# Kernel optimization log

Hardware: AMD Instinct MI355X
Metric: run time of the kernel (lower is better)

The kernel has to match this reference:

```python
import jax, jax.numpy as jnp
import numpy as np
import math

SCALES = (1, 2, 4, 8)


def interp1d(x, L_out):
    """F.interpolate(mode='linear', align_corners=False) along last axis."""
    L_in = x.shape[-1]
    if L_in == L_out:
        return x
    scale = L_in / L_out
    src = (jnp.arange(L_out, dtype=jnp.float32) + 0.5) * scale - 0.5
    src = jnp.clip(src, 0.0, float(L_in - 1))
    i0 = jnp.floor(src).astype(jnp.int32)
    i1 = jnp.minimum(i0 + 1, L_in - 1)
    w1 = (src - i0.astype(jnp.float32)).astype(x.dtype)
    return x[..., i0] * (1.0 - w1) + x[..., i1] * w1


def setup_inputs() -> dict:
    key = jax.random.key(0)
    ks = jax.random.split(key, 5)
    B, H, S, D = 2, 16, 1024, 64
    query = jax.random.normal(ks[0], (B, H, S, D), jnp.float32)
    k = jax.random.normal(ks[1], (B, H, S, D), jnp.float32)
    v = jax.random.normal(ks[2], (B, H, S, D), jnp.float32)
    # 4 per-scale Linear(head_dim, head_dim): W[i] is [out, in] (torch layout), b[i] is [out]
    W = jax.random.normal(ks[3], (len(SCALES), D, D), jnp.float32) * (1.0 / np.sqrt(D))
    b = jax.random.normal(ks[4], (len(SCALES), D), jnp.float32) * 0.01
    return {"query": query, "key": k, "value": v, "W": W, "b": b}


def reference(query, key, value, W, b):
    B, H, S, D = query.shape
    inv_sqrt_d = 1.0 / math.sqrt(D)
    outs, probs_all = [], []
    for i, s in enumerate(SCALES):
        if s > 1:
            # avg_pool1d(kernel=stride=s) over the sequence axis
            pk = key.reshape(B, H, S // s, s, D).mean(axis=3)
            pv = value.reshape(B, H, S // s, s, D).mean(axis=3)
        else:
            pk, pv = key, value
        # per-scale linear projection of pooled keys (torch Linear: x @ W.T + b)
        proj = jnp.einsum('bhkd,ed->bhke', pk, W[i]) + b[i]
        scores = jnp.einsum('bhqd,bhkd->bhqk', query, proj) * inv_sqrt_d
        probs = jax.nn.softmax(scores, axis=-1)  # [B,H,S,S//s]
        if s > 1:
            # upsample attn probs along key axis, and pooled values along seq axis
            probs = interp1d(probs, S)                               # [B,H,S,S]
            pv = jnp.swapaxes(interp1d(jnp.swapaxes(pv, -1, -2), S), -1, -2)  # [B,H,S,D]
        outs.append(jnp.einsum('bhqk,bhkd->bhqd', probs, pv))
        probs_all.append(probs)
    combined_output = jnp.stack(outs).mean(axis=0)
    combined_attention = jnp.stack(probs_all).mean(axis=0)
    return combined_output, combined_attention
```

## Files before the change

### kernel.cpp

```cpp
#include <hip/hip_runtime.h>

#define S_LEN 1024
#define DH 64
#define NBH 32
#define CROWS 1920
#define HEAD_K (CROWS * DH)
#define NCHUNK (HEAD_K / 8)
#define ATTN_OFF (NBH * S_LEN * DH)
#define PSTR 1928

typedef __attribute__((ext_vector_type(8))) short bf8_t;
typedef __attribute__((ext_vector_type(4))) float f32x4_t;

__device__ __forceinline__ unsigned short f2bf(float x) {
  unsigned u = __float_as_uint(x);
  u += 0x7fffu + ((u >> 16) & 1u);
  return (unsigned short)(u >> 16);
}
__device__ __forceinline__ float bf2f(unsigned short h) {
  return __uint_as_float(((unsigned)h) << 16);
}

__global__ __launch_bounds__(256, 3) void prep_kernel(
    const float* __restrict__ key, const float* __restrict__ value,
    const float* __restrict__ W, const float* __restrict__ b,
    unsigned short* __restrict__ projB, unsigned short* __restrict__ mpvB)
{
  __shared__ __align__(16) float Wl[64 * 64];
  __shared__ __align__(16) float pkv[68 * 68];
  __shared__ __align__(16) float prL[64 * 68];
  __shared__ float coefs[64 * 4];
  const int t = threadIdx.x;
  const int bid = blockIdx.x;
  const int bh = bid / 30;
  const int tt = bid % 30;
  int si, jt;
  if (tt < 16)      { si = 0; jt = tt; }
  else if (tt < 24) { si = 1; jt = tt - 16; }
  else if (tt < 28) { si = 2; jt = tt - 24; }
  else              { si = 3; jt = tt - 28; }
  const int s = 1 << si;
  const int L = 1024 >> si;
  const int off = (si == 0) ? 0 : (si == 1) ? 1024 : (si == 2) ? 1536 : 1792;
  const int j0 = jt << 6;
  const float invs = 1.0f / (float)s;

  for (int i = t; i < 1024; i += 256)
    *(float4*)&Wl[i * 4] = *(const float4*)&W[si * 4096 + i * 4];

  const float* Kp = key + bh * (S_LEN * DH);
  for (int i = t; i < 1024; i += 256) {
    const int j = i >> 4, d4 = (i & 15) << 2;
    const float* src = Kp + (j0 + j) * s * DH + d4;
    float4 a = {0.f, 0.f, 0.f, 0.f};
    for (int f = 0; f < s; f++) {
      const float4 kv = *(const float4*)(src + f * DH);
      a.x += kv.x; a.y += kv.y; a.z += kv.z; a.w += kv.w;
    }
    a.x *= invs; a.y *= invs; a.z *= invs; a.w *= invs;
    *(float4*)&pkv[j * 68 + d4] = a;
  }

  if (t < 64) {
    const int j = j0 + t;
    float cm = 0.f, cc = 0.f, cp = 0.f;
    const int klo = max(0, (j - 1) * s);
    const int khi = min(S_LEN - 1, (j + 2) * s);
    for (int kf = klo; kf <= khi; kf++) {
      float srcp = ((float)kf + 0.5f) * invs - 0.5f;
      srcp = fminf(fmaxf(srcp, 0.f), (float)(L - 1));
      const int i0 = (int)floorf(srcp);
      const int i1 = min(i0 + 1, L - 1);
      const float w = srcp - (float)i0;
      float u = 0.f;
      if (i0 == j) u += 1.f - w;
      if (i1 == j) u += w;
      if (u != 0.f) {
        const float g0 = u * (1.f - w), g1 = u * w;
        if (i0 == j) cc += g0; else cm += g0;
        if (i1 == j) cc += g1; else cp += g1;
      }
    }
    coefs[t * 4 + 0] = cm; coefs[t * 4 + 1] = cc; coefs[t * 4 + 2] = cp;
  }
  __syncthreads();

  {
    const int j  = t & 63;
    const int e0 = (t >> 6) << 4;
    float acc[16];
    #pragma unroll
    for (int ee = 0; ee < 16; ee++) acc[ee] = b[si * 64 + e0 + ee];
    #pragma unroll
    for (int dq = 0; dq < 16; dq++) {
      const float4 p4 = *(const float4*)&pkv[j * 68 + dq * 4];
      #pragma unroll
      for (int ee = 0; ee < 16; ee++) {
        const float4 w4 = *(const float4*)&Wl[(e0 + ee) * 64 + dq * 4];
        acc[ee] += p4.x * w4.x + p4.y * w4.y + p4.z * w4.z + p4.w * w4.w;
      }
    }
    #pragma unroll
    for (int ee = 0; ee < 16; ee++) prL[j * 68 + e0 + ee] = acc[ee];
  }
  __syncthreads();

  const float* Vp = value + bh * (S_LEN * DH);
  for (int i = t; i < 1088; i += 256) {
    const int hj = i >> 4, d4 = (i & 15) << 2;
    const int jg = min(max(j0 - 2 + hj, 0), L - 1);
    const float* src = Vp + jg * s * DH + d4;
    float4 a = {0.f, 0.f, 0.f, 0.f};
    for (int f = 0; f < s; f++) {
      const float4 vv = *(const float4*)(src + f * DH);
      a.x += vv.x; a.y += vv.y; a.z += vv.z; a.w += vv.w;
    }
    a.x *= invs; a.y *= invs; a.z *= invs; a.w *= invs;
    *(float4*)&pkv[hj * 68 + d4] = a;
  }

  const int ktg0 = (off + j0) >> 4;
  for (int c = t; c < 512; c += 256) {
    const int ktl = c >> 7;
    const int db  = (c >> 6) & 1;
    const int ln  = c & 63;
    const int kl  = ktl * 16 + (ln & 15);
    const int e0p = db * 32 + ((ln >> 4) & 3) * 8;
    const float4 a  = *(const float4*)&prL[kl * 68 + e0p];
    const float4 c4 = *(const float4*)&prL[kl * 68 + e0p + 4];
    bf8_t v;
    v[0] = (short)f2bf(a.x);  v[1] = (short)f2bf(a.y);
    v[2] = (short)f2bf(a.z);  v[3] = (short)f2bf(a.w);
    v[4] = (short)f2bf(c4.x); v[5] = (short)f2bf(c4.y);
    v[6] = (short)f2bf(c4.z); v[7] = (short)f2bf(c4.w);
    ((bf8_t*)projB)[bh * NCHUNK + ((ktg0 + ktl) * 2 + db) * 64 + ln] = v;
  }
  __syncthreads();

  const int kbg0 = (off + j0) >> 5;
  for (int c = t; c < 512; c += 256) {
    const int kbl = c >> 8;
    const int nt  = (c >> 6) & 3;
    const int ln  = c & 63;
    const int d   = nt * 16 + (ln & 15);
    const int r0  = kbl * 32 + ((ln >> 4) & 3) * 8;
    bf8_t v;
    #pragma unroll
    for (int jj = 0; jj < 8; jj++) {
      const int rl = r0 + jj;
      const float cm = coefs[rl * 4 + 0];
      const float cc = coefs[rl * 4 + 1];
      const float cp = coefs[rl * 4 + 2];
      const float val = cm * pkv[(rl + 1) * 68 + d] +
                        cc * pkv[(rl + 2) * 68 + d] +
                        cp * pkv[(rl + 3) * 68 + d];
      v[jj] = (short)f2bf(val);
    }
    ((bf8_t*)mpvB)[bh * NCHUNK + ((kbg0 + kbl) * 4 + nt) * 64 + ln] = v;
  }
}

__global__ __launch_bounds__(256, 2) void fused_attn_kernel(
    const float* __restrict__ query, const unsigned short* __restrict__ projB,
    const unsigned short* __restrict__ mpvB, float* __restrict__ out)
{
  __shared__ __align__(16) unsigned short prbf[16 * PSTR];
  const int t    = threadIdx.x;
  const int bh   = blockIdx.x & 31;
  const int qt   = blockIdx.x >> 5;
  const int q0   = qt << 4;
  const int wave = t >> 6;
  const int lane = t & 63;
  const int quad = lane >> 4;
  const int n16  = lane & 15;

  bf8_t af0, af1;
  {
    const float* qrow = query + bh * (S_LEN * DH) + (q0 + n16) * DH;
    const float4 a0 = *(const float4*)(qrow + quad * 8);
    const float4 a1 = *(const float4*)(qrow + quad * 8 + 4);
    const float4 a2 = *(const float4*)(qrow + 32 + quad * 8);
    const float4 a3 = *(const float4*)(qrow + 32 + quad * 8 + 4);
    af0[0] = (short)f2bf(a0.x); af0[1] = (short)f2bf(a0.y);
    af0[2] = (short)f2bf(a0.z); af0[3] = (short)f2bf(a0.w);
    af0[4] = (short)f2bf(a1.x); af0[5] = (short)f2bf(a1.y);
    af0[6] = (short)f2bf(a1.z); af0[7] = (short)f2bf(a1.w);
    af1[0] = (short)f2bf(a2.x); af1[1] = (short)f2bf(a2.y);
    af1[2] = (short)f2bf(a2.z); af1[3] = (short)f2bf(a2.w);
    af1[4] = (short)f2bf(a3.x); af1[5] = (short)f2bf(a3.y);
    af1[6] = (short)f2bf(a3.z); af1[7] = (short)f2bf(a3.w);
  }

  {
    const bf8_t* pB = (const bf8_t*)projB + bh * NCHUNK;
    for (int kt = wave; kt < 120; kt += 4) {
      const bf8_t b0 = pB[(kt * 2 + 0) * 64 + lane];
      const bf8_t b1 = pB[(kt * 2 + 1) * 64 + lane];
      f32x4_t c = {0.f, 0.f, 0.f, 0.f};
      c = __builtin_amdgcn_mfma_f32_16x16x32_bf16(af0, b0, c, 0, 0, 0);
      c = __builtin_amdgcn_mfma_f32_16x16x32_bf16(af1, b1, c, 0, 0, 0);
      const int col = kt * 16 + n16;
      #pragma unroll
      for (int i = 0; i < 4; i++)
        prbf[(quad * 4 + i) * PSTR + col] = f2bf(c[i] * 0.125f);
    }
  }
  __syncthreads();

  {
    const int rr = t >> 4;
    const int g  = t & 15;
    unsigned short* prr = prbf + rr * PSTR;
    #pragma unroll
    for (int si = 0; si < 4; si++) {
      const int L   = 1024 >> si;
      const int off = (si == 0) ? 0 : (si == 1) ? 1024 : (si == 2) ? 1536 : 1792;
      const int nch = L >> 2;
      float m = -1e30f;
      for (int ch = g; ch < nch; ch += 16) {
        const ushort4 u = *(const ushort4*)(prr + off + ch * 4);
        m = fmaxf(m, fmaxf(fmaxf(bf2f(u.x), bf2f(u.y)),
                           fmaxf(bf2f(u.z), bf2f(u.w))));
      }
      #pragma unroll
      for (int dlt = 8; dlt >= 1; dlt >>= 1) m = fmaxf(m, __shfl_xor(m, dlt));
      float ssum = 0.f;
      for (int ch = g; ch < nch; ch += 16) {
        ushort4 u = *(const ushort4*)(prr + off + ch * 4);
        const float e0 = __expf(bf2f(u.x) - m);
        const float e1 = __expf(bf2f(u.y) - m);
        const float e2 = __expf(bf2f(u.z) - m);
        const float e3 = __expf(bf2f(u.w) - m);
        ssum += (e0 + e1) + (e2 + e3);
        u.x = f2bf(e0); u.y = f2bf(e1); u.z = f2bf(e2); u.w = f2bf(e3);
        *(ushort4*)(prr + off + ch * 4) = u;
      }
      #pragma unroll
      for (int dlt = 8; dlt >= 1; dlt >>= 1) ssum += __shfl_xor(ssum, dlt);
      const float inv = 1.0f / ssum;
      for (int ch = g; ch < nch; ch += 16) {
        ushort4 u = *(const ushort4*)(prr + off + ch * 4);
        u.x = f2bf(bf2f(u.x) * inv); u.y = f2bf(bf2f(u.y) * inv);
        u.z = f2bf(bf2f(u.z) * inv); u.w = f2bf(bf2f(u.w) * inv);
        *(ushort4*)(prr + off + ch * 4) = u;
      }
    }
  }
  __syncthreads();

  {
    const bf8_t* pM = (const bf8_t*)mpvB + bh * NCHUNK;
    f32x4_t acc = {0.f, 0.f, 0.f, 0.f};
    for (int kb = 0; kb < 60; kb++) {
      const bf8_t a = *(const bf8_t*)(prbf + n16 * PSTR + kb * 32 + quad * 8);
      const bf8_t bb = pM[(kb * 4 + wave) * 64 + lane];
      acc = __builtin_amdgcn_mfma_f32_16x16x32_bf16(a, bb, acc, 0, 0, 0);
    }
    float* ob = out + bh * (S_LEN * DH) + q0 * DH;
    #pragma unroll
    for (int i = 0; i < 4; i++)
      ob[(quad * 4 + i) * DH + wave * 16 + n16] = acc[i] * 0.25f;
  }

  float* ab = out + ATTN_OFF + (size_t)bh * (S_LEN * S_LEN) + (size_t)q0 * S_LEN;
  for (int rep = 0; rep < 16; rep++) {
    const int idx = rep * 256 + t;
    const int rr  = idx >> 8;
    const int k0  = (idx & 255) << 2;
    const unsigned short* p2 = prbf + rr * PSTR;
    const ushort4 bs = *(const ushort4*)(p2 + k0);
    float res[4] = {bf2f(bs.x), bf2f(bs.y), bf2f(bs.z), bf2f(bs.w)};
    #pragma unroll
    for (int si = 1; si < 4; si++) {
      const int   L     = 1024 >> si;
      const int   off2  = (si == 1) ? 1024 : (si == 2) ? 1536 : 1792;
      const float inv_s = (si == 1) ? 0.5f : (si == 2) ? 0.25f : 0.125f;
      #pragma unroll
      for (int kk = 0; kk < 4; kk++) {
        float srcp = ((float)(k0 + kk) + 0.5f) * inv_s - 0.5f;
        srcp = fminf(fmaxf(srcp, 0.f), (float)(L - 1));
        const int i0 = (int)floorf(srcp);
        const int i1 = min(i0 + 1, L - 1);
        const float w = srcp - (float)i0;
        res[kk] += (1.f - w) * bf2f(p2[off2 + i0]) + w * bf2f(p2[off2 + i1]);
      }
    }
    *(float4*)(ab + (size_t)idx * 4) =
        make_float4(res[0] * 0.25f, res[1] * 0.25f,
                    res[2] * 0.25f, res[3] * 0.25f);
  }
}

extern "C" void kernel_launch(void* const* d_in, const int* in_sizes, int n_in,
                              void* d_out, int out_size, void* d_ws, size_t ws_size,
                              hipStream_t stream) {
  (void)in_sizes; (void)n_in; (void)out_size; (void)ws_size;
  const float* query = (const float*)d_in[0];
  const float* key   = (const float*)d_in[1];
  const float* value = (const float*)d_in[2];
  const float* W     = (const float*)d_in[3];
  const float* b     = (const float*)d_in[4];
  float* out = (float*)d_out;

  unsigned short* projB = (unsigned short*)d_ws;
  unsigned short* mpvB  = projB + (size_t)NBH * HEAD_K;

  prep_kernel<<<NBH * 30, 256, 0, stream>>>(key, value, W, b, projB, mpvB);
  fused_attn_kernel<<<NBH * 64, 256, 0, stream>>>(query, projB, mpvB, out);
}
```

Measured before the change: 310.5 us.

## Restructure prep kernel: templated scales, direct W reads, fewer LDS stages and barriers

```diff
diff --git a/kernel.cpp b/kernel.cpp
--- a/kernel.cpp
+++ b/kernel.cpp
@@ -21,44 +21,54 @@
   return __uint_as_float(((unsigned)h) << 16);
 }
 
-__global__ __launch_bounds__(256, 3) void prep_kernel(
+template<int SI>
+__device__ __forceinline__ void prep_body(
     const float* __restrict__ key, const float* __restrict__ value,
     const float* __restrict__ W, const float* __restrict__ b,
-    unsigned short* __restrict__ projB, unsigned short* __restrict__ mpvB)
+    unsigned short* __restrict__ projB, unsigned short* __restrict__ mpvB,
+    const int bh, const int jt, const int t,
+    float* __restrict__ pkK, float* __restrict__ pkV, float* __restrict__ coefs)
 {
-  __shared__ __align__(16) float Wl[64 * 64];
-  __shared__ __align__(16) float pkv[68 * 68];
-  __shared__ __align__(16) float prL[64 * 68];
-  __shared__ float coefs[64 * 4];
-  const int t = threadIdx.x;
-  const int bid = blockIdx.x;
-  const int bh = bid / 30;
-  const int tt = bid % 30;
-  int si, jt;
-  if (tt < 16)      { si = 0; jt = tt; }
-  else if (tt < 24) { si = 1; jt = tt - 16; }
-  else if (tt < 28) { si = 2; jt = tt - 24; }
-  else              { si = 3; jt = tt - 28; }
-  const int s = 1 << si;
-  const int L = 1024 >> si;
-  const int off = (si == 0) ? 0 : (si == 1) ? 1024 : (si == 2) ? 1536 : 1792;
+  constexpr int   s    = 1 << SI;
+  constexpr int   L    = 1024 >> SI;
+  constexpr int   off  = (SI == 0) ? 0 : (SI == 1) ? 1024 : (SI == 2) ? 1536 : 1792;
+  constexpr float invs = 1.0f / (float)s;
   const int j0 = jt << 6;
-  const float invs = 1.0f / (float)s;
-
-  for (int i = t; i < 1024; i += 256)
-    *(float4*)&Wl[i * 4] = *(const float4*)&W[si * 4096 + i * 4];
 
   const float* Kp = key + bh * (S_LEN * DH);
-  for (int i = t; i < 1024; i += 256) {
+  const float* Vp = value + bh * (S_LEN * DH);
+
+  #pragma unroll
+  for (int it = 0; it < 4; it++) {
+    const int i = it * 256 + t;
     const int j = i >> 4, d4 = (i & 15) << 2;
     const float* src = Kp + (j0 + j) * s * DH + d4;
     float4 a = {0.f, 0.f, 0.f, 0.f};
+    #pragma unroll
     for (int f = 0; f < s; f++) {
       const float4 kv = *(const float4*)(src + f * DH);
       a.x += kv.x; a.y += kv.y; a.z += kv.z; a.w += kv.w;
     }
     a.x *= invs; a.y *= invs; a.z *= invs; a.w *= invs;
-    *(float4*)&pkv[j * 68 + d4] = a;
+    *(float4*)&pkK[j * 68 + d4] = a;
+  }
+
+  #pragma unroll
+  for (int it = 0; it < 5; it++) {
+    const int i = it * 256 + t;
+    if (i < 1088) {
+      const int hj = i >> 4, d4 = (i & 15) << 2;
+      const int jg = min(max(j0 - 2 + hj, 0), L - 1);
+      const float* src = Vp + jg * s * DH + d4;
+      float4 a = {0.f, 0.f, 0.f, 0.f};
+      #pragma unroll
+      for (int f = 0; f < s; f++) {
+        const float4 vv = *(const float4*)(src + f * DH);
+        a.x += vv.x; a.y += vv.y; a.z += vv.z; a.w += vv.w;
+      }
+      a.x *= invs; a.y *= invs; a.z *= invs; a.w *= invs;
+      *(float4*)&pkV[hj * 68 + d4] = a;
+    }
   }
 
   if (t < 64) {
@@ -87,58 +97,37 @@
 
   {
     const int j  = t & 63;
-    const int e0 = (t >> 6) << 4;
+    const int e0 = __builtin_amdgcn_readfirstlane((t >> 6) << 4);
+    const float* Wp = W + SI * 4096;
     float acc[16];
     #pragma unroll
-    for (int ee = 0; ee < 16; ee++) acc[ee] = b[si * 64 + e0 + ee];
+    for (int ee = 0; ee < 16; ee++) acc[ee] = b[SI * 64 + e0 + ee];
     #pragma unroll
     for (int dq = 0; dq < 16; dq++) {
-      const float4 p4 = *(const float4*)&pkv[j * 68 + dq * 4];
+      const float4 p4 = *(const float4*)&pkK[j * 68 + dq * 4];
       #pragma unroll
       for (int ee = 0; ee < 16; ee++) {
-        const float4 w4 = *(const float4*)&Wl[(e0 + ee) * 64 + dq * 4];
+        const float4 w4 = *(const float4*)&Wp[(e0 + ee) * 64 + dq * 4];
         acc[ee] += p4.x * w4.x + p4.y * w4.y + p4.z * w4.z + p4.w * w4.w;
       }
     }
-    #pragma unroll
-    for (int ee = 0; ee < 16; ee++) prL[j * 68 + e0 + ee] = acc[ee];
-  }
-  __syncthreads();
-
-  const float* Vp = value + bh * (S_LEN * DH);
-  for (int i = t; i < 1088; i += 256) {
-    const int hj = i >> 4, d4 = (i & 15) << 2;
-    const int jg = min(max(j0 - 2 + hj, 0), L - 1);
-    const float* src = Vp + jg * s * DH + d4;
-    float4 a = {0.f, 0.f, 0.f, 0.f};
-    for (int f = 0; f < s; f++) {
-      const float4 vv = *(const float4*)(src + f * DH);
-      a.x += vv.x; a.y += vv.y; a.z += vv.z; a.w += vv.w;
-    }
-    a.x *= invs; a.y *= invs; a.z *= invs; a.w *= invs;
-    *(float4*)&pkv[hj * 68 + d4] = a;
-  }
-
-  const int ktg0 = (off + j0) >> 4;
-  for (int c = t; c < 512; c += 256) {
-    const int ktl = c >> 7;
-    const int db  = (c >> 6) & 1;
-    const int ln  = c & 63;
-    const int kl  = ktl * 16 + (ln & 15);
-    const int e0p = db * 32 + ((ln >> 4) & 3) * 8;
-    const float4 a  = *(const float4*)&prL[kl * 68 + e0p];
-    const float4 c4 = *(const float4*)&prL[kl * 68 + e0p + 4];
-    bf8_t v;
-    v[0] = (short)f2bf(a.x);  v[1] = (short)f2bf(a.y);
-    v[2] = (short)f2bf(a.z);  v[3] = (short)f2bf(a.w);
-    v[4] = (short)f2bf(c4.x); v[5] = (short)f2bf(c4.y);
-    v[6] = (short)f2bf(c4.z); v[7] = (short)f2bf(c4.w);
-    ((bf8_t*)projB)[bh * NCHUNK + ((ktg0 + ktl) * 2 + db) * 64 + ln] = v;
-  }
-  __syncthreads();
+    const int ktg0 = (off + j0) >> 4;
+    const int ktl  = j >> 4;
+    #pragma unroll
+    for (int h = 0; h < 2; h++) {
+      const int e0p = e0 + h * 8;
+      const int ln  = (((e0p >> 3) & 3) << 4) | (j & 15);
+      bf8_t v;
+      #pragma unroll
+      for (int jj = 0; jj < 8; jj++) v[jj] = (short)f2bf(acc[h * 8 + jj]);
+      ((bf8_t*)projB)[bh * NCHUNK + ((ktg0 + ktl) * 2 + (e0p >> 5)) * 64 + ln] = v;
+    }
+  }
 
   const int kbg0 = (off + j0) >> 5;
-  for (int c = t; c < 512; c += 256) {
+  #pragma unroll
+  for (int cc2 = 0; cc2 < 2; cc2++) {
+    const int c   = cc2 * 256 + t;
     const int kbl = c >> 8;
     const int nt  = (c >> 6) & 3;
     const int ln  = c & 63;
@@ -148,16 +137,35 @@
     #pragma unroll
     for (int jj = 0; jj < 8; jj++) {
       const int rl = r0 + jj;
-      const float cm = coefs[rl * 4 + 0];
-      const float cc = coefs[rl * 4 + 1];
-      const float cp = coefs[rl * 4 + 2];
-      const float val = cm * pkv[(rl + 1) * 68 + d] +
-                        cc * pkv[(rl + 2) * 68 + d] +
-                        cp * pkv[(rl + 3) * 68 + d];
+      const float val = coefs[rl * 4 + 0] * pkV[(rl + 1) * 68 + d] +
+                        coefs[rl * 4 + 1] * pkV[(rl + 2) * 68 + d] +
+                        coefs[rl * 4 + 2] * pkV[(rl + 3) * 68 + d];
       v[jj] = (short)f2bf(val);
     }
     ((bf8_t*)mpvB)[bh * NCHUNK + ((kbg0 + kbl) * 4 + nt) * 64 + ln] = v;
   }
+}
+
+__global__ __launch_bounds__(256, 4) void prep_kernel(
+    const float* __restrict__ key, const float* __restrict__ value,
+    const float* __restrict__ W, const float* __restrict__ b,
+    unsigned short* __restrict__ projB, unsigned short* __restrict__ mpvB)
+{
+  __shared__ __align__(16) float pkK[64 * 68];
+  __shared__ __align__(16) float pkV[68 * 68];
+  __shared__ float coefs[64 * 4];
+  const int t = threadIdx.x;
+  const int bid = blockIdx.x;
+  const int bh = bid / 30;
+  const int tt = bid % 30;
+  if (tt < 16)
+    prep_body<0>(key, value, W, b, projB, mpvB, bh, tt, t, pkK, pkV, coefs);
+  else if (tt < 24)
+    prep_body<1>(key, value, W, b, projB, mpvB, bh, tt - 16, t, pkK, pkV, coefs);
+  else if (tt < 28)
+    prep_body<2>(key, value, W, b, projB, mpvB, bh, tt - 24, t, pkK, pkV, coefs);
+  else
+    prep_body<3>(key, value, W, b, projB, mpvB, bh, tt - 28, t, pkK, pkV, coefs);
 }
 
 __global__ __launch_bounds__(256, 2) void fused_attn_kernel(
```

After: 307.8 us. Within noise of the previous version (-0.9%).
